# Kernel optimization log

Measured on AMD Instinct MI355X. Metric: run time of the kernel, lower is better.

The kernel has to match this reference:

```python
import jax, jax.numpy as jnp
import numpy as np

B, T, D, H, C = 8, 512, 1024, 16, 10   # batch, seq (T_out+1), d=nb_lon*nb_lat, heads, classes
L = 4                                   # effective layers = n - 1 (ModuleLists hold n-1 entries)
DH = D // H
RD = float(np.sqrt(D))
EPS = 1e-5


def make_pos():
    # pos[t, 2k] = sin((t+1)*w_k), pos[t, 2k+1] = sin((t+1)*w_k + pi/2)
    t = np.arange(1, T + 1, dtype=np.float32)[:, None]          # [T,1]
    kk = np.arange(D // 2, dtype=np.float32)
    omega = np.repeat(1.0 / 1000.0 ** (2.0 * kk / D), 2)[None]  # [1,D]
    phase = np.tile(np.array([0.0, np.pi / 2], dtype=np.float32), D // 2)[None]
    return jnp.asarray(np.sin(t * omega + phase), dtype=jnp.float32)


def setup_inputs() -> dict:
    key = jax.random.key(0)
    ks = jax.random.split(key, 12)
    s = 0.02
    inp = {
        'x': jax.random.normal(ks[0], (B, T, D), jnp.float32),
        'k': jax.random.normal(ks[1], (B, H, T, DH), jnp.float32),
        'v': jax.random.normal(ks[2], (B, H, T, DH), jnp.float32),
        'pos': make_pos(),
        'Wq1': jax.random.normal(ks[3], (L, D, D), jnp.float32) * s,
        'Wk1': jax.random.normal(ks[4], (L, D, D), jnp.float32) * s,
        'Wv1': jax.random.normal(ks[5], (L, D, D), jnp.float32) * s,
        'Wq2': jax.random.normal(ks[6], (L, D, D), jnp.float32) * s,
        'Wfc': jax.random.normal(ks[7], (L, D, D), jnp.float32) * s,
        'bfc': jnp.zeros((L, D), jnp.float32),
        'g1': jnp.ones((L - 1, D), jnp.float32),
        'b1': jnp.zeros((L - 1, D), jnp.float32),
        'g2': jnp.ones((L, D), jnp.float32),
        'b2': jnp.zeros((L, D), jnp.float32),
        'g3': jnp.ones((L, D), jnp.float32),
        'b3': jnp.zeros((L, D), jnp.float32),
        # xavier_uniform on [1, C-1]
        'cutoff': jax.random.uniform(ks[8], (1, C - 1), jnp.float32,
                                     -np.sqrt(6.0 / C), np.sqrt(6.0 / C)),
    }
    return inp


def _ln(x, g, b):
    m = jnp.mean(x, axis=-1, keepdims=True)
    var = jnp.var(x, axis=-1, keepdims=True)
    return (x - m) / jnp.sqrt(var + EPS) * g + b


def _self_attn(x, Wq, Wk, Wv):
    # nn.Linear: y = x @ W.T ; no causal mask (masking defaults to False)
    q = (x @ Wq.T).reshape(B, T, H, DH)
    kk = (x @ Wk.T).reshape(B, T, H, DH)
    vv = (x @ Wv.T).reshape(B, T, H, DH)
    a = jnp.einsum('bqhe,bkhe->bhqk', q, kk) / RD
    a = jax.nn.softmax(a, axis=-1)
    o = jnp.einsum('bhqk,bkhe->bqhe', a, vv).reshape(B, T, D)
    return x + o


def _cross_attn(x, Wq, k, v, mask):
    q = (x @ Wq.T).reshape(B, T, H, DH)
    a = jnp.einsum('bqhe,bhke->bhqk', q, k) / RD
    a = jnp.where(mask, -jnp.inf, a)  # causal mask on cross scores (intended semantics)
    a = jax.nn.softmax(a, axis=-1)
    o = jnp.einsum('bhqk,bhke->bqhe', a, v).reshape(B, T, D)
    return x + o


def reference(x, k, v, pos, Wq1, Wk1, Wv1, Wq2, Wfc, bfc,
              g1, b1, g2, b2, g3, b3, cutoff):
    x = x + pos
    mask = jnp.triu(jnp.ones((T, T), bool), 1)
    for i in range(L):
        if i != 0:
            x = _ln(x, g1[i - 1], b1[i - 1])
        x = _self_attn(x, Wq1[i], Wk1[i], Wv1[i])
        x = _ln(x, g2[i], b2[i])
        x = _cross_attn(x, Wq2[i], k, v, mask)
        x = _ln(x, g3[i], b3[i])
        x = jax.nn.relu(x @ Wfc[i].T + bfc[i]) + x
    # ordinal sigmoid head: cumulative cutoffs, adjacent sigmoid differences
    b = jnp.cumsum(jnp.concatenate([cutoff[:, :1], cutoff[:, 1:] ** 2], axis=1), axis=1)  # [1,C-1]
    sig = jax.nn.sigmoid(b[0] - x[..., None])  # [B,T,D,C-1]
    probs = jnp.concatenate(
        [sig[..., :1], sig[..., 1:] - sig[..., :-1], 1.0 - sig[..., -1:]], axis=-1)
    return probs
```

## Files before the change

kernel.cpp:

```cpp
#include <hip/hip_runtime.h>


#define BB   8
#define TT   512
#define DD   1024
#define HH   16
#define DHH  64
#define LLAY 4
#define MM   (BB*TT)
#define MD   ((size_t)MM*DD)
#define INV_RD (1.0f/32.0f)
#define LNEPS 1e-5f

typedef unsigned short ushort_t;
typedef __attribute__((ext_vector_type(8))) short short8;
typedef __attribute__((ext_vector_type(4))) float floatx4;

__device__ inline ushort_t f2bf(float f) {
  unsigned u = __builtin_bit_cast(unsigned, f);
  unsigned r = (u + 0x7FFFu + ((u >> 16) & 1u)) >> 16;
  return (ushort_t)r;
}

__global__ __launch_bounds__(256) void cast_all_k(
    const float* __restrict__ Wq1, const float* __restrict__ Wk1,
    const float* __restrict__ Wv1, const float* __restrict__ Wq2f,
    const float* __restrict__ Wfcf, const float* __restrict__ kin,
    const float* __restrict__ vin,
    ushort_t* __restrict__ wqkv, ushort_t* __restrict__ wq2,
    ushort_t* __restrict__ wfc, ushort_t* __restrict__ kinbf,
    ushort_t* __restrict__ vinbf) {
  int seg = blockIdx.x >> 12;
  size_t j = ((size_t)(blockIdx.x & 4095)) * 256 + threadIdx.x;
  const float* src;
  switch (seg) {
    case 0: src = Wq1; break;
    case 1: src = Wk1; break;
    case 2: src = Wv1; break;
    case 3: src = Wq2f; break;
    case 4: src = Wfcf; break;
    case 5: src = kin; break;
    default: src = vin; break;
  }
  float4 v = ((const float4*)src)[j];
  ushort4 o; o.x = f2bf(v.x); o.y = f2bf(v.y); o.z = f2bf(v.z); o.w = f2bf(v.w);
  if (seg < 3) {
    int d4 = (int)(j & 255);
    int n  = (int)((j >> 8) & 1023);
    int i  = (int)(j >> 18);
    size_t drow = (size_t)i * 3072 + (size_t)seg * 1024 + n;
    ((ushort4*)wqkv)[drow * 256 + d4] = o;
  } else {
    ushort_t* dst = (seg == 3) ? wq2 : (seg == 4) ? wfc : (seg == 5) ? kinbf : vinbf;
    ((ushort4*)dst)[j] = o;
  }
}

__global__ __launch_bounds__(256) void add_pos_k(const float* __restrict__ x,
                                                 const float* __restrict__ pos,
                                                 float* __restrict__ out,
                                                 ushort_t* __restrict__ out_bf) {
  size_t i = (size_t)blockIdx.x * 256 + threadIdx.x;
  int dq  = (int)(i & 255);
  int row = (int)(i >> 8);
  int t   = row & (TT - 1);
  float4 a = ((const float4*)x)[i];
  float4 p = ((const float4*)pos)[(size_t)t * 256 + dq];
  a.x += p.x; a.y += p.y; a.z += p.z; a.w += p.w;
  ((float4*)out)[i] = a;
  ushort4 b; b.x = f2bf(a.x); b.y = f2bf(a.y); b.z = f2bf(a.z); b.w = f2bf(a.w);
  ((ushort4*)out_bf)[i] = b;
}

__global__ __launch_bounds__(256) void ln_k(const float* __restrict__ in,
                                            float* __restrict__ out,
                                            ushort_t* __restrict__ out_bf,
                                            const float* __restrict__ g,
                                            const float* __restrict__ bt) {
  int row = blockIdx.x;
  int t = threadIdx.x;
  const float4* r4 = (const float4*)(in + (size_t)row * DD);
  float4 v = r4[t];
  float s  = v.x + v.y + v.z + v.w;
  float ss = v.x*v.x + v.y*v.y + v.z*v.z + v.w*v.w;
#pragma unroll
  for (int off = 32; off > 0; off >>= 1) {
    s  += __shfl_down(s, off);
    ss += __shfl_down(ss, off);
  }
  __shared__ float red[8];
  int w = t >> 6;
  if ((t & 63) == 0) { red[w] = s; red[4 + w] = ss; }
  __syncthreads();
  s  = red[0] + red[1] + red[2] + red[3];
  ss = red[4] + red[5] + red[6] + red[7];
  float mean = s * (1.0f / DD);
  float var  = ss * (1.0f / DD) - mean * mean;
  float inv  = rsqrtf(var + LNEPS);
  float4 gv = ((const float4*)g)[t];
  float4 bv = ((const float4*)bt)[t];
  float4 o;
  o.x = (v.x - mean) * inv * gv.x + bv.x;
  o.y = (v.y - mean) * inv * gv.y + bv.y;
  o.z = (v.z - mean) * inv * gv.z + bv.z;
  o.w = (v.w - mean) * inv * gv.w + bv.w;
  ((float4*)(out + (size_t)row * DD))[t] = o;
  ushort4 ob; ob.x = f2bf(o.x); ob.y = f2bf(o.y); ob.z = f2bf(o.z); ob.w = f2bf(o.w);
  ((ushort4*)(out_bf + (size_t)row * DD))[t] = ob;
}

__global__ __launch_bounds__(256) void gemm_mfma_bt_k(const ushort_t* __restrict__ A,
                                                      const ushort_t* __restrict__ W,
                                                      void* __restrict__ Cout,
                                                      const float* __restrict__ bias,
                                                      const float* __restrict__ lnres,
                                                      int mode) {
  __shared__ ushort_t As[128 * 32];
  __shared__ ushort_t Bs[128 * 32];
  int t = threadIdx.x;
  int n0 = blockIdx.x * 128, m0 = blockIdx.y * 128;
  int lane = t & 63, w = t >> 6;
  int wm = (w >> 1) * 64, wn = (w & 1) * 64;
  int fr = lane & 15, q = lane >> 4;
  const short8* ap[4]; const short8* bp[4];
#pragma unroll
  for (int i = 0; i < 4; i++) {
    int r  = wm + i * 16 + fr;
    int rn = wn + i * 16 + fr;
    ap[i] = (const short8*)(As + r  * 32 + ((q ^ ((r  >> 1) & 3)) * 8));
    bp[i] = (const short8*)(Bs + rn * 32 + ((q ^ ((rn >> 1) & 3)) * 8));
  }
  auto* As3 = (__attribute__((address_space(3))) ushort_t*)As;
  auto* Bs3 = (__attribute__((address_space(3))) ushort_t*)Bs;
  floatx4 acc[4][4] = {};
  for (int k0 = 0; k0 < DD; k0 += 32) {
    __syncthreads();
#pragma unroll
    for (int j = 0; j < 2; j++) {
      int e = t + j * 256;
      int row = e >> 2, slot = e & 3;
      int c = slot ^ ((row >> 1) & 3);
      const ushort_t* asrc = A + (size_t)(m0 + row) * DD + k0 + c * 8;
      const ushort_t* wsrc = W + (size_t)(n0 + row) * DD + k0 + c * 8;
      __builtin_amdgcn_global_load_lds(
          (const __attribute__((address_space(1))) unsigned*)asrc,
          (__attribute__((address_space(3))) unsigned*)(As3 + e * 8), 16, 0, 0);
      __builtin_amdgcn_global_load_lds(
          (const __attribute__((address_space(1))) unsigned*)wsrc,
          (__attribute__((address_space(3))) unsigned*)(Bs3 + e * 8), 16, 0, 0);
    }
    __syncthreads();
    short8 af[4], bf[4];
#pragma unroll
    for (int i = 0; i < 4; i++) { af[i] = *ap[i]; bf[i] = *bp[i]; }
#pragma unroll
    for (int i = 0; i < 4; i++)
#pragma unroll
      for (int j = 0; j < 4; j++)
        acc[i][j] = __builtin_amdgcn_mfma_f32_16x16x32_bf16(af[i], bf[j], acc[i][j], 0, 0, 0);
  }
  int orow = m0 + wm + q * 4;
  int ocol = n0 + wn + fr;
  if (mode == 1) {
    int seg = n0 >> 10;
    ushort_t* Cb = (ushort_t*)Cout + (size_t)seg * MD;
#pragma unroll
    for (int i = 0; i < 4; i++)
#pragma unroll
      for (int j = 0; j < 4; j++)
#pragma unroll
        for (int rr = 0; rr < 4; rr++)
          Cb[(size_t)(orow + i * 16 + rr) * DD + ((ocol + j * 16) & 1023)] =
              f2bf(acc[i][j][rr]);
  } else {
    float* C = (float*)Cout;
#pragma unroll
    for (int j = 0; j < 4; j++) {
      int colg = ocol + j * 16;
      float bv = bias[colg];
#pragma unroll
      for (int i = 0; i < 4; i++)
#pragma unroll
        for (int rr = 0; rr < 4; rr++) {
          size_t idx = (size_t)(orow + i * 16 + rr) * DD + colg;
          C[idx] = fmaxf(acc[i][j][rr] + bv, 0.f) + lnres[idx];
        }
    }
  }
}

__global__ __launch_bounds__(256) void attn_mfma_k(const ushort_t* __restrict__ Qb,
                                                   const ushort_t* __restrict__ Kb,
                                                   const ushort_t* __restrict__ Vb,
                                                   const float* __restrict__ resid,
                                                   float* __restrict__ out,
                                                   int cross) {
  __shared__ ushort_t Qs[64 * 64];
  __shared__ ushort_t Ks[64 * 64];
  __shared__ ushort_t Vts[64 * 64];
  __shared__ ushort_t Ps[4 * 16 * 64];
  int t = threadIdx.x, lane = t & 63, w = t >> 6;
  int fr = lane & 15, q8 = lane >> 4;
  int qt = blockIdx.x, bh = blockIdx.y;
  int b = bh >> 4, h = bh & 15;
  size_t qbase = ((size_t)(b * TT + qt * 64)) * DD + h * DHH;
  size_t kvbase; int kvstride;
  if (cross) { kvbase = (size_t)bh * TT * DHH;          kvstride = DHH; }
  else       { kvbase = (size_t)b * TT * DD + h * DHH;  kvstride = DD;  }

  auto* Qs3  = (__attribute__((address_space(3))) ushort_t*)Qs;
  auto* Ks3  = (__attribute__((address_space(3))) ushort_t*)Ks;

#pragma unroll
  for (int j = 0; j < 2; j++) {
    int e = t + j * 256;
    int row = e >> 3, slot = e & 7;
    int c = slot ^ (row & 7);
    const ushort_t* src = Qb + qbase + (size_t)row * DD + c * 8;
    __builtin_amdgcn_global_load_lds(
        (const __attribute__((address_space(1))) unsigned*)src,
        (__attribute__((address_space(3))) unsigned*)(Qs3 + e * 8), 16, 0, 0);
  }
  __syncthreads();

  short8 qf[2];
#pragma unroll
  for (int ks = 0; ks < 2; ks++) {
    int row = w * 16 + fr;
    int slot = (ks * 4 + q8) ^ (row & 7);
    qf[ks] = *(const short8*)(Qs + row * 64 + slot * 8);
  }

  float m_i[4], l_i[4];
  floatx4 o_acc[4] = {};
#pragma unroll
  for (int r = 0; r < 4; r++) { m_i[r] = -1e30f; l_i[r] = 0.f; }

  int nch = cross ? (qt + 1) : 8;
  for (int ch = 0; ch < nch; ch++) {
    __syncthreads();
#pragma unroll
    for (int j = 0; j < 2; j++) {
      int e = t + j * 256;
      int row = e >> 3, slot = e & 7;
      int c = slot ^ (row & 7);
      const ushort_t* src = Kb + kvbase + (size_t)(ch * 64 + row) * kvstride + c * 8;
      __builtin_amdgcn_global_load_lds(
          (const __attribute__((address_space(1))) unsigned*)src,
          (__attribute__((address_space(3))) unsigned*)(Ks3 + e * 8), 16, 0, 0);
    }
    {
      int kp = t & 31, dhg = (t >> 5) * 8;
      const ushort_t* v0 = Vb + kvbase + (size_t)(ch * 64 + 2 * kp) * kvstride + dhg;
      short8 a0 = *(const short8*)v0;
      short8 a1 = *(const short8*)(v0 + kvstride);
#pragma unroll
      for (int j = 0; j < 8; j++) {
        int dh = dhg + j;
        int slot = (kp >> 2) ^ (dh & 7);
        unsigned pk = (unsigned)(unsigned short)a0[j] |
                      ((unsigned)(unsigned short)a1[j] << 16);
        *(unsigned*)(Vts + dh * 64 + slot * 8 + (kp & 3) * 2) = pk;
      }
    }
    __syncthreads();

    floatx4 s[4] = {};
    __builtin_amdgcn_s_setprio(1);
#pragma unroll
    for (int nt = 0; nt < 4; nt++) {
      int key = nt * 16 + fr;
#pragma unroll
      for (int ks = 0; ks < 2; ks++) {
        int slot = (ks * 4 + q8) ^ (key & 7);
        short8 kf = *(const short8*)(Ks + key * 64 + slot * 8);
        s[nt] = __builtin_amdgcn_mfma_f32_16x16x32_bf16(qf[ks], kf, s[nt], 0, 0, 0);
      }
    }
    __builtin_amdgcn_s_setprio(0);
    float sv[4][4];
#pragma unroll
    for (int nt = 0; nt < 4; nt++)
#pragma unroll
      for (int r = 0; r < 4; r++)
        sv[nt][r] = s[nt][r] * INV_RD;
    if (cross && ch == qt) {
#pragma unroll
      for (int nt = 0; nt < 4; nt++) {
        int key_g = ch * 64 + nt * 16 + fr;
#pragma unroll
        for (int r = 0; r < 4; r++) {
          int q_g = qt * 64 + w * 16 + q8 * 4 + r;
          if (key_g > q_g) sv[nt][r] = -1e30f;
        }
      }
    }

    float pv[4][4];
#pragma unroll
    for (int r = 0; r < 4; r++) {
      float mch = fmaxf(fmaxf(sv[0][r], sv[1][r]), fmaxf(sv[2][r], sv[3][r]));
#pragma unroll
      for (int off = 1; off < 16; off <<= 1) mch = fmaxf(mch, __shfl_xor(mch, off));
      float mn = fmaxf(m_i[r], mch);
      float alpha = __expf(m_i[r] - mn);
      m_i[r] = mn;
      float rs = 0.f;
#pragma unroll
      for (int nt = 0; nt < 4; nt++) {
        float pe = __expf(sv[nt][r] - mn);
        pv[nt][r] = pe; rs += pe;
      }
#pragma unroll
      for (int off = 1; off < 16; off <<= 1) rs += __shfl_xor(rs, off);
      l_i[r] = l_i[r] * alpha + rs;
#pragma unroll
      for (int nt = 0; nt < 4; nt++) o_acc[nt][r] *= alpha;
    }

    ushort_t* Pw = Ps + w * 1024;
#pragma unroll
    for (int nt = 0; nt < 4; nt++) {
      int col = nt * 16 + fr;
#pragma unroll
      for (int r = 0; r < 4; r++) {
        int row = q8 * 4 + r;
        int slot = (col >> 3) ^ (row & 7);
        Pw[row * 64 + slot * 8 + (col & 7)] = f2bf(pv[nt][r]);
      }
    }
    short8 pf[2];
#pragma unroll
    for (int ks = 0; ks < 2; ks++) {
      int slot = (ks * 4 + q8) ^ (fr & 7);
      pf[ks] = *(const short8*)(Pw + fr * 64 + slot * 8);
    }
    __builtin_amdgcn_s_setprio(1);
#pragma unroll
    for (int nt = 0; nt < 4; nt++) {
      int dh = nt * 16 + fr;
#pragma unroll
      for (int ks = 0; ks < 2; ks++) {
        int slot = (ks * 4 + q8) ^ (dh & 7);
        short8 vf = *(const short8*)(Vts + dh * 64 + slot * 8);
        o_acc[nt] = __builtin_amdgcn_mfma_f32_16x16x32_bf16(pf[ks], vf, o_acc[nt], 0, 0, 0);
      }
    }
    __builtin_amdgcn_s_setprio(0);
  }

  float invl[4];
#pragma unroll
  for (int r = 0; r < 4; r++) invl[r] = 1.0f / l_i[r];
#pragma unroll
  for (int nt = 0; nt < 4; nt++) {
#pragma unroll
    for (int r = 0; r < 4; r++) {
      size_t row_g = (size_t)(b * TT + qt * 64 + w * 16 + q8 * 4 + r);
      size_t idx = row_g * DD + h * DHH + nt * 16 + fr;
      out[idx] = resid[idx] + o_acc[nt][r] * invl[r];
    }
  }
}

__global__ __launch_bounds__(256) void head_k(const float* __restrict__ x,
                                              const float* __restrict__ cut,
                                              float* __restrict__ out) {
  __shared__ float obuf[2560];
  int t = threadIdx.x;
  size_t e = (size_t)blockIdx.x * 256 + t;
  float xv = x[e];
  float bj = cut[0];
  float sprev = 1.0f / (1.0f + __expf(xv - bj));
  obuf[t * 10 + 0] = sprev;
#pragma unroll
  for (int j = 1; j < 9; j++) {
    float cj = cut[j];
    bj += cj * cj;
    float sj = 1.0f / (1.0f + __expf(xv - bj));
    obuf[t * 10 + j] = sj - sprev;
    sprev = sj;
  }
  obuf[t * 10 + 9] = 1.0f - sprev;
  __syncthreads();
  size_t base = (size_t)blockIdx.x * 2560;
#pragma unroll
  for (int r = 0; r < 10; r++) out[base + r * 256 + t] = obuf[r * 256 + t];
}

extern "C" void kernel_launch(void* const* d_in, const int* in_sizes, int n_in,
                              void* d_out, int out_size, void* d_ws, size_t ws_size,
                              hipStream_t stream) {
  (void)in_sizes; (void)n_in; (void)out_size; (void)ws_size;
  const float* x    = (const float*)d_in[0];
  const float* kin  = (const float*)d_in[1];
  const float* vin  = (const float*)d_in[2];
  const float* pos  = (const float*)d_in[3];
  const float* Wq1  = (const float*)d_in[4];
  const float* Wk1  = (const float*)d_in[5];
  const float* Wv1  = (const float*)d_in[6];
  const float* Wq2  = (const float*)d_in[7];
  const float* Wfc  = (const float*)d_in[8];
  const float* bfc  = (const float*)d_in[9];
  const float* g1   = (const float*)d_in[10];
  const float* b1   = (const float*)d_in[11];
  const float* g2   = (const float*)d_in[12];
  const float* b2   = (const float*)d_in[13];
  const float* g3   = (const float*)d_in[14];
  const float* b3   = (const float*)d_in[15];
  const float* cut  = (const float*)d_in[16];
  float* out = (float*)d_out;

  float* cur = (float*)d_ws;
  float* tmp = cur + MD;
  ushort_t* act_bf = (ushort_t*)(tmp + MD);
  ushort_t* qbf    = act_bf + MD;
  ushort_t* kbf    = qbf + MD;
  ushort_t* vbf    = kbf + MD;
  ushort_t* kinbf  = vbf + MD;
  ushort_t* vinbf  = kinbf + MD;
  ushort_t* wqkv   = vinbf + MD;
  ushort_t* wq2    = wqkv + (size_t)LLAY * 3 * DD * DD;
  ushort_t* wfc    = wq2  + (size_t)LLAY * DD * DD;

  dim3 b256(256);
  dim3 gqkv(3 * DD / 128, MM / 128);
  dim3 gg(DD / 128, MM / 128);
  dim3 ga(TT / 64, BB * HH);

  cast_all_k<<<7 * 4096, b256, 0, stream>>>(Wq1, Wk1, Wv1, Wq2, Wfc, kin, vin,
                                            wqkv, wq2, wfc, kinbf, vinbf);

  add_pos_k<<<MD / 1024, b256, 0, stream>>>(x, pos, cur, act_bf);

  for (int i = 0; i < LLAY; i++) {
    const float* attn_in;
    if (i) {
      ln_k<<<MM, b256, 0, stream>>>(cur, tmp, act_bf,
                                    g1 + (size_t)(i - 1) * DD, b1 + (size_t)(i - 1) * DD);
      attn_in = tmp;
    } else {
      attn_in = cur;
    }
    gemm_mfma_bt_k<<<gqkv, b256, 0, stream>>>(act_bf, wqkv + (size_t)i * 3 * DD * DD,
                                              qbf, nullptr, nullptr, 1);
    attn_mfma_k<<<ga, b256, 0, stream>>>(qbf, kbf, vbf, attn_in, cur, 0);

    ln_k<<<MM, b256, 0, stream>>>(cur, tmp, act_bf,
                                  g2 + (size_t)i * DD, b2 + (size_t)i * DD);
    gemm_mfma_bt_k<<<gg, b256, 0, stream>>>(act_bf, wq2 + (size_t)i * DD * DD,
                                            qbf, nullptr, nullptr, 1);
    attn_mfma_k<<<ga, b256, 0, stream>>>(qbf, kinbf, vinbf, tmp, cur, 1);

    ln_k<<<MM, b256, 0, stream>>>(cur, tmp, act_bf,
                                  g3 + (size_t)i * DD, b3 + (size_t)i * DD);
    gemm_mfma_bt_k<<<gg, b256, 0, stream>>>(act_bf, wfc + (size_t)i * DD * DD,
                                            cur, bfc + (size_t)i * DD, tmp, 2);
  }

  head_k<<<MD / 256, b256, 0, stream>>>(cur, cut, out);
}
```

Before: 1.160 ms.

## Use 128x64 GEMM tiles for DxD projections, swizzle block order across XCDs

Adds a 128x64-tile GEMM for the two 1024-wide projections, raising the grid from 256 to 512 blocks so the 256 CUs are better filled. The QKV GEMM and both attention kernels now use 1D grids remapped so blocks that share data land on the same XCD, which should improve L2 reuse. The add-pos kernel is folded into the cast kernel as an extra segment, saving one launch. Smaller tiles lower arithmetic intensity per block.

Result: faster. 978.9 us (-15.6%).

```diff
diff --git a/kernel.cpp b/kernel.cpp
--- a/kernel.cpp
+++ b/kernel.cpp
@@ -26,12 +26,26 @@
     const float* __restrict__ Wq1, const float* __restrict__ Wk1,
     const float* __restrict__ Wv1, const float* __restrict__ Wq2f,
     const float* __restrict__ Wfcf, const float* __restrict__ kin,
-    const float* __restrict__ vin,
+    const float* __restrict__ vin, const float* __restrict__ x,
+    const float* __restrict__ pos,
     ushort_t* __restrict__ wqkv, ushort_t* __restrict__ wq2,
     ushort_t* __restrict__ wfc, ushort_t* __restrict__ kinbf,
-    ushort_t* __restrict__ vinbf) {
+    ushort_t* __restrict__ vinbf, float* __restrict__ cur,
+    ushort_t* __restrict__ act_bf) {
   int seg = blockIdx.x >> 12;
   size_t j = ((size_t)(blockIdx.x & 4095)) * 256 + threadIdx.x;
+  if (seg == 7) {
+    int dq  = (int)(j & 255);
+    int row = (int)(j >> 8);
+    int t   = row & (TT - 1);
+    float4 a = ((const float4*)x)[j];
+    float4 p = ((const float4*)pos)[(size_t)t * 256 + dq];
+    a.x += p.x; a.y += p.y; a.z += p.z; a.w += p.w;
+    ((float4*)cur)[j] = a;
+    ushort4 b; b.x = f2bf(a.x); b.y = f2bf(a.y); b.z = f2bf(a.z); b.w = f2bf(a.w);
+    ((ushort4*)act_bf)[j] = b;
+    return;
+  }
   const float* src;
   switch (seg) {
     case 0: src = Wq1; break;
@@ -54,22 +68,6 @@
     ushort_t* dst = (seg == 3) ? wq2 : (seg == 4) ? wfc : (seg == 5) ? kinbf : vinbf;
     ((ushort4*)dst)[j] = o;
   }
-}
-
-__global__ __launch_bounds__(256) void add_pos_k(const float* __restrict__ x,
-                                                 const float* __restrict__ pos,
-                                                 float* __restrict__ out,
-                                                 ushort_t* __restrict__ out_bf) {
-  size_t i = (size_t)blockIdx.x * 256 + threadIdx.x;
-  int dq  = (int)(i & 255);
-  int row = (int)(i >> 8);
-  int t   = row & (TT - 1);
-  float4 a = ((const float4*)x)[i];
-  float4 p = ((const float4*)pos)[(size_t)t * 256 + dq];
-  a.x += p.x; a.y += p.y; a.z += p.z; a.w += p.w;
-  ((float4*)out)[i] = a;
-  ushort4 b; b.x = f2bf(a.x); b.y = f2bf(a.y); b.z = f2bf(a.z); b.w = f2bf(a.w);
-  ((ushort4*)out_bf)[i] = b;
 }
 
 __global__ __launch_bounds__(256) void ln_k(const float* __restrict__ in,
@@ -111,14 +109,16 @@
 
 __global__ __launch_bounds__(256) void gemm_mfma_bt_k(const ushort_t* __restrict__ A,
                                                       const ushort_t* __restrict__ W,
-                                                      void* __restrict__ Cout,
-                                                      const float* __restrict__ bias,
-                                                      const float* __restrict__ lnres,
-                                                      int mode) {
+                                                      ushort_t* __restrict__ Cout,
+                                                      int nbx) {
   __shared__ ushort_t As[128 * 32];
   __shared__ ushort_t Bs[128 * 32];
   int t = threadIdx.x;
-  int n0 = blockIdx.x * 128, m0 = blockIdx.y * 128;
+  int d = blockIdx.x;
+  int chunk = gridDim.x >> 3;
+  int logical = (d & 7) * chunk + (d >> 3);
+  int bx = logical % nbx, by = logical / nbx;
+  int n0 = bx * 128, m0 = by * 128;
   int lane = t & 63, w = t >> 6;
   int wm = (w >> 1) * 64, wn = (w & 1) * 64;
   int fr = lane & 15, q = lane >> 4;
@@ -161,22 +161,98 @@
   }
   int orow = m0 + wm + q * 4;
   int ocol = n0 + wn + fr;
+  int seg = n0 >> 10;
+  ushort_t* Cb = Cout + (size_t)seg * MD;
+#pragma unroll
+  for (int i = 0; i < 4; i++)
+#pragma unroll
+    for (int j = 0; j < 4; j++)
+#pragma unroll
+      for (int rr = 0; rr < 4; rr++)
+        Cb[(size_t)(orow + i * 16 + rr) * DD + ((ocol + j * 16) & 1023)] =
+            f2bf(acc[i][j][rr]);
+}
+
+__global__ __launch_bounds__(256) void gemm64_k(const ushort_t* __restrict__ A,
+                                                const ushort_t* __restrict__ W,
+                                                void* __restrict__ Cout,
+                                                const float* __restrict__ bias,
+                                                const float* __restrict__ lnres,
+                                                int mode) {
+  __shared__ ushort_t As[128 * 32];
+  __shared__ ushort_t Bs[64 * 32];
+  int t = threadIdx.x;
+  int d = blockIdx.x;
+  int logical = (d & 7) * 64 + (d >> 3);
+  int bx = logical & 15, by = logical >> 4;
+  int n0 = bx * 64, m0 = by * 128;
+  int lane = t & 63, w = t >> 6;
+  int wm = (w >> 1) * 64, wn = (w & 1) * 32;
+  int fr = lane & 15, q = lane >> 4;
+  const short8* ap[4]; const short8* bp[2];
+#pragma unroll
+  for (int i = 0; i < 4; i++) {
+    int r = wm + i * 16 + fr;
+    ap[i] = (const short8*)(As + r * 32 + ((q ^ ((r >> 1) & 3)) * 8));
+  }
+#pragma unroll
+  for (int j = 0; j < 2; j++) {
+    int rn = wn + j * 16 + fr;
+    bp[j] = (const short8*)(Bs + rn * 32 + ((q ^ ((rn >> 1) & 3)) * 8));
+  }
+  auto* As3 = (__attribute__((address_space(3))) ushort_t*)As;
+  auto* Bs3 = (__attribute__((address_space(3))) ushort_t*)Bs;
+  floatx4 acc[4][2] = {};
+  for (int k0 = 0; k0 < DD; k0 += 32) {
+    __syncthreads();
+#pragma unroll
+    for (int j = 0; j < 2; j++) {
+      int e = t + j * 256;
+      int row = e >> 2, slot = e & 3;
+      int c = slot ^ ((row >> 1) & 3);
+      const ushort_t* asrc = A + (size_t)(m0 + row) * DD + k0 + c * 8;
+      __builtin_amdgcn_global_load_lds(
+          (const __attribute__((address_space(1))) unsigned*)asrc,
+          (__attribute__((address_space(3))) unsigned*)(As3 + e * 8), 16, 0, 0);
+    }
+    {
+      int e = t;
+      int row = e >> 2, slot = e & 3;
+      int c = slot ^ ((row >> 1) & 3);
+      const ushort_t* wsrc = W + (size_t)(n0 + row) * DD + k0 + c * 8;
+      __builtin_amdgcn_global_load_lds(
+          (const __attribute__((address_space(1))) unsigned*)wsrc,
+          (__attribute__((address_space(3))) unsigned*)(Bs3 + e * 8), 16, 0, 0);
+    }
+    __syncthreads();
+    short8 af[4], bf[2];
+#pragma unroll
+    for (int i = 0; i < 4; i++) af[i] = *ap[i];
+#pragma unroll
+    for (int j = 0; j < 2; j++) bf[j] = *bp[j];
+#pragma unroll
+    for (int i = 0; i < 4; i++)
+#pragma unroll
+      for (int j = 0; j < 2; j++)
+        acc[i][j] = __builtin_amdgcn_mfma_f32_16x16x32_bf16(af[i], bf[j], acc[i][j], 0, 0, 0);
+  }
+  int orow = m0 + wm + q * 4;
   if (mode == 1) {
-    int seg = n0 >> 10;
-    ushort_t* Cb = (ushort_t*)Cout + (size_t)seg * MD;
+    ushort_t* Cb = (ushort_t*)Cout;
 #pragma unroll
     for (int i = 0; i < 4; i++)
 #pragma unroll
-      for (int j = 0; j < 4; j++)
+      for (int j = 0; j < 2; j++) {
+        int colg = n0 + wn + j * 16 + fr;
 #pragma unroll
         for (int rr = 0; rr < 4; rr++)
-          Cb[(size_t)(orow + i * 16 + rr) * DD + ((ocol + j * 16) & 1023)] =
-              f2bf(acc[i][j][rr]);
+          Cb[(size_t)(orow + i * 16 + rr) * DD + colg] = f2bf(acc[i][j][rr]);
+      }
   } else {
     float* C = (float*)Cout;
 #pragma unroll
-    for (int j = 0; j < 4; j++) {
-      int colg = ocol + j * 16;
+    for (int j = 0; j < 2; j++) {
+      int colg = n0 + wn + j * 16 + fr;
       float bv = bias[colg];
 #pragma unroll
       for (int i = 0; i < 4; i++)
@@ -201,7 +277,9 @@
   __shared__ ushort_t Ps[4 * 16 * 64];
   int t = threadIdx.x, lane = t & 63, w = t >> 6;
   int fr = lane & 15, q8 = lane >> 4;
-  int qt = blockIdx.x, bh = blockIdx.y;
+  int dsp = blockIdx.x;
+  int logical = (dsp & 7) * 128 + (dsp >> 3);
+  int qt = logical & 7, bh = logical >> 3;
   int b = bh >> 4, h = bh & 15;
   size_t qbase = ((size_t)(b * TT + qt * 64)) * DD + h * DHH;
   size_t kvbase; int kvstride;
@@ -424,14 +502,10 @@
   ushort_t* wfc    = wq2  + (size_t)LLAY * DD * DD;
 
   dim3 b256(256);
-  dim3 gqkv(3 * DD / 128, MM / 128);
-  dim3 gg(DD / 128, MM / 128);
-  dim3 ga(TT / 64, BB * HH);
-
-  cast_all_k<<<7 * 4096, b256, 0, stream>>>(Wq1, Wk1, Wv1, Wq2, Wfc, kin, vin,
-                                            wqkv, wq2, wfc, kinbf, vinbf);
-
-  add_pos_k<<<MD / 1024, b256, 0, stream>>>(x, pos, cur, act_bf);
+
+  cast_all_k<<<8 * 4096, b256, 0, stream>>>(Wq1, Wk1, Wv1, Wq2, Wfc, kin, vin,
+                                            x, pos, wqkv, wq2, wfc, kinbf, vinbf,
+                                            cur, act_bf);
 
   for (int i = 0; i < LLAY; i++) {
     const float* attn_in;
@@ -442,20 +516,20 @@
     } else {
       attn_in = cur;
     }
-    gemm_mfma_bt_k<<<gqkv, b256, 0, stream>>>(act_bf, wqkv + (size_t)i * 3 * DD * DD,
-                                              qbf, nullptr, nullptr, 1);
-    attn_mfma_k<<<ga, b256, 0, stream>>>(qbf, kbf, vbf, attn_in, cur, 0);
+    gemm_mfma_bt_k<<<768, b256, 0, stream>>>(act_bf, wqkv + (size_t)i * 3 * DD * DD,
+                                             qbf, 24);
+    attn_mfma_k<<<1024, b256, 0, stream>>>(qbf, kbf, vbf, attn_in, cur, 0);
 
     ln_k<<<MM, b256, 0, stream>>>(cur, tmp, act_bf,
                                   g2 + (size_t)i * DD, b2 + (size_t)i * DD);
-    gemm_mfma_bt_k<<<gg, b256, 0, stream>>>(act_bf, wq2 + (size_t)i * DD * DD,
-                                            qbf, nullptr, nullptr, 1);
-    attn_mfma_k<<<ga, b256, 0, stream>>>(qbf, kinbf, vinbf, tmp, cur, 1);
+    gemm64_k<<<512, b256, 0, stream>>>(act_bf, wq2 + (size_t)i * DD * DD,
+                                       qbf, nullptr, nullptr, 1);
+    attn_mfma_k<<<1024, b256, 0, stream>>>(qbf, kinbf, vinbf, tmp, cur, 1);
 
     ln_k<<<MM, b256, 0, stream>>>(cur, tmp, act_bf,
                                   g3 + (size_t)i * DD, b3 + (size_t)i * DD);
-    gemm_mfma_bt_k<<<gg, b256, 0, stream>>>(act_bf, wfc + (size_t)i * DD * DD,
-                                            cur, bfc + (size_t)i * DD, tmp, 2);
+    gemm64_k<<<512, b256, 0, stream>>>(act_bf, wfc + (size_t)i * DD * DD,
+                                       cur, bfc + (size_t)i * DD, tmp, 2);
   }
 
   head_k<<<MD / 256, b256, 0, stream>>>(cur, cut, out);
```
